# Optimization experiments

Measured on AMD Instinct MI355X. Metric: run time of the kernel, lower is better.

## Reference

```python
import jax, jax.numpy as jnp
import numpy as np

S, L, E, H, HID, T = 4096, 16, 256, 512, 512, 50
CHAR_V = 128


def _lstm_scan(x, W_ih, W_hh, b):
    """x: [T, B, D] -> all hidden states [T, B, H]. PyTorch gate order i,f,g,o.
    b is the sum of torch's b_ih + b_hh (identical math)."""
    Hh = W_hh.shape[1]
    B = x.shape[1]

    def cell(carry, xt):
        h, c = carry
        g = xt @ W_ih.T + h @ W_hh.T + b  # [B, 4H]
        i, f, gg, o = jnp.split(g, 4, axis=-1)
        c = jax.nn.sigmoid(f) * c + jax.nn.sigmoid(i) * jnp.tanh(gg)
        h = jax.nn.sigmoid(o) * jnp.tanh(c)
        return (h, c), h

    init = (jnp.zeros((B, Hh), x.dtype), jnp.zeros((B, Hh), x.dtype))
    _, hs = jax.lax.scan(cell, init, x)
    return hs


def setup_inputs() -> dict:
    key = jax.random.key(0)
    ks = jax.random.split(key, 18)

    def p(k, shape):
        return jax.random.normal(k, shape, jnp.float32) * 0.05

    return {
        "chars": jax.random.randint(ks[0], (S, L), 0, CHAR_V),
        "char_lens": jax.random.randint(ks[1], (S,), 0, L),
        "char_table": p(ks[2], (CHAR_V, E)),
        "cW_ih": p(ks[3], (4 * E, E)),
        "cW_hh": p(ks[4], (4 * E, E)),
        "cb": p(ks[5], (4 * E,)),
        "W_ih0": p(ks[6], (2, 4 * H, E)),
        "W_hh0": p(ks[7], (2, 4 * H, H)),
        "b0": p(ks[8], (2, 4 * H)),
        "W_ih1": p(ks[9], (2, 4 * H, 2 * H)),
        "W_hh1": p(ks[10], (2, 4 * H, H)),
        "b1": p(ks[11], (2, 4 * H)),
        "fc1_w": p(ks[12], (HID, 2 * H)),
        "fc1_b": p(ks[13], (HID,)),
        "fc2_w": p(ks[14], (T, HID)),
        "fc2_b": p(ks[15], (T,)),
    }


def reference(chars, char_lens, char_table, cW_ih, cW_hh, cb,
              W_ih0, W_hh0, b0, W_ih1, W_hh1, b1,
              fc1_w, fc1_b, fc2_w, fc2_b):
    n_words = chars.shape[0]
    # --- char LSTM: batched over all words (replaces per-word python loop) ---
    emb = char_table[chars]                               # [S, L, E]
    hs = _lstm_scan(emb.transpose(1, 0, 2), cW_ih, cW_hh, cb)  # [L, S, E]
    lens = jnp.maximum(char_lens, 1)                      # every word has >=1 char
    word_emb = hs[lens - 1, jnp.arange(n_words)]          # hn per word: [S, E]

    # --- 2-layer bidirectional sentence LSTM, batch = 1 ---
    x = word_emb[:, None, :]                              # [S, 1, E]

    def bi_layer(x, Wih, Whh, b):
        fwd = _lstm_scan(x, Wih[0], Whh[0], b[0])
        bwd = _lstm_scan(x[::-1], Wih[1], Whh[1], b[1])[::-1]
        return jnp.concatenate([fwd, bwd], axis=-1)       # [S, 1, 2H]

    x = bi_layer(x, W_ih0, W_hh0, b0)
    x = bi_layer(x, W_ih1, W_hh1, b1)

    # --- MLP head ---
    out = x[:, 0, :]                                      # [S, 2H]
    out = jnp.tanh(out @ fc1_w.T + fc1_b)                 # [S, HID]
    return out @ fc2_w.T + fc2_b                          # [S, T]
```

## Files before the change

kernel.cpp:

```cpp
#include <hip/hip_runtime.h>
#include <math.h>
#include <stdint.h>


#define NPOS 4096
#define GDIM 2048

__device__ __forceinline__ float sigf(float x) { return 1.0f / (1.0f + __expf(-x)); }
__device__ __forceinline__ float tanh_fast(float x) {
  float e = __expf(2.f * x);
  return 1.f - 2.f / (e + 1.f);
}

__global__ __launch_bounds__(256) void build_wt_kernel(
    const float* __restrict__ cWih, const float* __restrict__ cWhh,
    float* __restrict__ Wt)
{
  __shared__ float tile[64][65];
  const int k0 = blockIdx.x * 64;
  const int g0 = blockIdx.y * 64;
  const float* src = (k0 < 256) ? cWih : cWhh;
  const int sk0 = k0 & 255;
  for (int i = threadIdx.x; i < 64 * 64; i += 256) {
    int r = i >> 6, cc = i & 63;
    tile[r][cc] = src[(size_t)(g0 + r) * 256 + sk0 + cc];
  }
  __syncthreads();
  for (int i = threadIdx.x; i < 64 * 64; i += 256) {
    int kk = i >> 6, gg = i & 63;
    Wt[(size_t)(k0 + kk) * 1024 + g0 + gg] = tile[gg][kk];
  }
}

__global__ __launch_bounds__(256) void char_lstm_kernel(
    const int* __restrict__ chars, const int* __restrict__ lens,
    const float* __restrict__ table, const float* __restrict__ Wt,
    const float* __restrict__ cb, float* __restrict__ word_emb)
{
  __shared__ float u[16][512];
  __shared__ float wt[8][1024];
  __shared__ int sidx[16];
  const int tid = threadIdx.x;
  const int ch = tid;
  const int w0 = blockIdx.x * 16;
  if (tid < 16) { int l = lens[w0 + tid]; sidx[tid] = (l < 1 ? 1 : l) - 1; }
  float c[16], acc0[16], acc1[16], acc2[16], acc3[16];
  #pragma unroll
  for (int w = 0; w < 16; ++w) { u[w][256 + ch] = 0.f; c[w] = 0.f; }
  const float cb0 = cb[ch], cb1 = cb[256 + ch], cb2 = cb[512 + ch], cb3 = cb[768 + ch];

  for (int t = 0; t < 16; ++t) {
    for (int w = 0; w < 16; ++w) {
      int cid = chars[(w0 + w) * 16 + t];
      u[w][ch] = table[(size_t)cid * 256 + ch];
    }
    #pragma unroll
    for (int w = 0; w < 16; ++w) { acc0[w] = cb0; acc1[w] = cb1; acc2[w] = cb2; acc3[w] = cb3; }
    for (int k0 = 0; k0 < 512; k0 += 8) {
      #pragma unroll
      for (int r = 0; r < 8; ++r)
        ((float4*)&wt[r][0])[tid] = ((const float4*)(Wt + (size_t)(k0 + r) * 1024))[tid];
      __syncthreads();
      #pragma unroll
      for (int kk = 0; kk < 8; ++kk) {
        const float wv0 = wt[kk][ch], wv1 = wt[kk][256 + ch];
        const float wv2 = wt[kk][512 + ch], wv3 = wt[kk][768 + ch];
        #pragma unroll
        for (int w = 0; w < 16; ++w) {
          const float uv = u[w][k0 + kk];
          acc0[w] = fmaf(wv0, uv, acc0[w]);
          acc1[w] = fmaf(wv1, uv, acc1[w]);
          acc2[w] = fmaf(wv2, uv, acc2[w]);
          acc3[w] = fmaf(wv3, uv, acc3[w]);
        }
      }
      __syncthreads();
    }
    #pragma unroll
    for (int w = 0; w < 16; ++w) {
      float iv = sigf(acc0[w]), fv = sigf(acc1[w]);
      float gv = tanhf(acc2[w]), ov = sigf(acc3[w]);
      c[w] = fv * c[w] + iv * gv;
      float h = ov * tanhf(c[w]);
      u[w][256 + ch] = h;
      if (t == sidx[w]) word_emb[(size_t)(w0 + w) * 256 + ch] = h;
    }
  }
}

template <int SPLIT, int ACT>
__global__ __launch_bounds__(256) void gemm_kernel(
    const float* __restrict__ A, const float* __restrict__ A2,
    const float* __restrict__ B, const float* __restrict__ bias,
    float* __restrict__ C, int M, int N, int K)
{
  __shared__ float At[8][132];
  __shared__ float Bt[8][132];
  const int tid = threadIdx.x;
  const int bm0 = blockIdx.x * 128, bn0 = blockIdx.y * 128;
  float acc[8][8];
  #pragma unroll
  for (int i = 0; i < 8; ++i)
    #pragma unroll
    for (int j = 0; j < 8; ++j) acc[i][j] = 0.f;
  const int sr = tid >> 1;
  const int sk = (tid & 1) * 4;
  const int tm = (tid >> 4) * 8, tn = (tid & 15) * 8;
  for (int k0 = 0; k0 < K; k0 += 8) {
    const int kg = k0 + sk;
    float4 av;
    if (SPLIT) {
      const float* srcp = (kg < 512) ? A : A2;
      av = *(const float4*)(srcp + (size_t)(bm0 + sr) * 512 + (kg & 511));
    } else {
      av = *(const float4*)(A + (size_t)(bm0 + sr) * K + kg);
    }
    float4 bv = {0.f, 0.f, 0.f, 0.f};
    if (bn0 + sr < N) bv = *(const float4*)(B + (size_t)(bn0 + sr) * K + kg);
    At[sk + 0][sr] = av.x; At[sk + 1][sr] = av.y; At[sk + 2][sr] = av.z; At[sk + 3][sr] = av.w;
    Bt[sk + 0][sr] = bv.x; Bt[sk + 1][sr] = bv.y; Bt[sk + 2][sr] = bv.z; Bt[sk + 3][sr] = bv.w;
    __syncthreads();
    #pragma unroll
    for (int kk = 0; kk < 8; ++kk) {
      float a[8], b[8];
      *(float4*)&a[0] = *(const float4*)&At[kk][tm];
      *(float4*)&a[4] = *(const float4*)&At[kk][tm + 4];
      *(float4*)&b[0] = *(const float4*)&Bt[kk][tn];
      *(float4*)&b[4] = *(const float4*)&Bt[kk][tn + 4];
      #pragma unroll
      for (int i = 0; i < 8; ++i)
        #pragma unroll
        for (int j = 0; j < 8; ++j) acc[i][j] = fmaf(a[i], b[j], acc[i][j]);
    }
    __syncthreads();
  }
  #pragma unroll
  for (int i = 0; i < 8; ++i) {
    const int m = bm0 + tm + i;
    float* crow = C + (size_t)m * N;
    #pragma unroll
    for (int j = 0; j < 8; ++j) {
      const int n = bn0 + tn + j;
      if (n < N) {
        float v = acc[i][j] + bias[n];
        if (ACT) v = tanhf(v);
        crow[n] = v;
      }
    }
  }
}

__global__ __launch_bounds__(512) void scan_kernel(
    const float* __restrict__ Xf, const float* __restrict__ Xb,
    const float* __restrict__ Whf, const float* __restrict__ Whb,
    unsigned long long* __restrict__ Tf, unsigned long long* __restrict__ Tb,
    float* __restrict__ Hf, float* __restrict__ Hb)
{
  __shared__ float lds_h[2][576];
  const int tid = threadIdx.x;
  const int dir = blockIdx.x & 1;
  const int wg  = blockIdx.x >> 1;
  const float* X = dir ? Xb : Xf;
  const float* Wh = dir ? Whb : Whf;
  unsigned long long* T = dir ? Tb : Tf;
  float* Hd = dir ? Hb : Hf;

  const int row8 = tid >> 3;
  const int klane = tid & 7;
  const int u = row8 >> 2, g = row8 & 3;
  const int R = g * 512 + wg * 16 + u;

  float wreg[64];
  {
    const float* wrow = Wh + (size_t)R * 512 + klane * 64;
    #pragma unroll
    for (int i = 0; i < 16; ++i) {
      float4 v = ((const float4*)wrow)[i];
      wreg[4 * i] = v.x; wreg[4 * i + 1] = v.y; wreg[4 * i + 2] = v.z; wreg[4 * i + 3] = v.w;
    }
  }
  const int l0 = 72 * klane;
  const int l1 = l0 + 36;
  const int la = tid + ((tid >> 5) << 2);

  for (int i = tid; i < 576; i += 512) lds_h[0][i] = 0.f;

  const bool xl = (klane == 0);
  float xcur = 0.f, xnxt = 0.f;
  if (xl) {
    xcur = X[(size_t)(dir ? NPOS - 1 : 0) * GDIM + R];
    xnxt = X[(size_t)(dir ? NPOS - 2 : 1) * GDIM + R];
  }
  float creg = 0.f;
  __syncthreads();

  for (int s = 0; s < NPOS; ++s) {
    const int p = dir ? (NPOS - 1 - s) : s;
    if (s > 0) {
      const unsigned int tg = (unsigned int)s;
      const unsigned long long* w = T + (size_t)((s - 1) & 1) * 512 + tid;
      unsigned long long v;
      do { v = __hip_atomic_load(w, __ATOMIC_RELAXED, __HIP_MEMORY_SCOPE_AGENT); }
      while ((unsigned int)(v >> 32) != tg);
      lds_h[s & 1][la] = __uint_as_float((unsigned int)v);
    }
    __syncthreads();
    const float* hb = &lds_h[s & 1][0];
    float sum = xl ? xcur : 0.f;
    if (xl) {
      xcur = xnxt;
      if (s + 2 < NPOS) xnxt = X[(size_t)(dir ? NPOS - 3 - s : s + 2) * GDIM + R];
    }
    #pragma unroll
    for (int i = 0; i < 8; ++i) {
      float4 a = *(const float4*)&hb[l0 + 4 * i];
      sum = fmaf(wreg[4 * i + 0], a.x, sum);
      sum = fmaf(wreg[4 * i + 1], a.y, sum);
      sum = fmaf(wreg[4 * i + 2], a.z, sum);
      sum = fmaf(wreg[4 * i + 3], a.w, sum);
    }
    #pragma unroll
    for (int i = 0; i < 8; ++i) {
      float4 a = *(const float4*)&hb[l1 + 4 * i];
      sum = fmaf(wreg[32 + 4 * i + 0], a.x, sum);
      sum = fmaf(wreg[32 + 4 * i + 1], a.y, sum);
      sum = fmaf(wreg[32 + 4 * i + 2], a.z, sum);
      sum = fmaf(wreg[32 + 4 * i + 3], a.w, sum);
    }
    sum += __shfl_xor(sum, 1);
    sum += __shfl_xor(sum, 2);
    sum += __shfl_xor(sum, 4);
    const int base = (tid & 63) & ~31;
    float gf = __shfl(sum, base + 8);
    float gg = __shfl(sum, base + 16);
    float go = __shfl(sum, base + 24);
    if ((tid & 31) == 0) {
      float iv = sigf(sum), fv = sigf(gf), gv = tanh_fast(gg), ov = sigf(go);
      creg = fv * creg + iv * gv;
      float h = ov * tanh_fast(creg);
      const int j = wg * 16 + u;
      unsigned long long pack = ((unsigned long long)(unsigned int)(s + 1) << 32)
                              | (unsigned long long)__float_as_uint(h);
      __hip_atomic_store(&T[(size_t)(s & 1) * 512 + j], pack,
                         __ATOMIC_RELAXED, __HIP_MEMORY_SCOPE_AGENT);
      Hd[(size_t)p * 512 + j] = h;
    }
  }
}

extern "C" void kernel_launch(void* const* d_in, const int* in_sizes, int n_in,
                              void* d_out, int out_size, void* d_ws, size_t ws_size,
                              hipStream_t stream) {
  const int* chars = (const int*)d_in[0];
  const int* lens = (const int*)d_in[1];
  const float* table = (const float*)d_in[2];
  const float* cWih = (const float*)d_in[3];
  const float* cWhh = (const float*)d_in[4];
  const float* cb = (const float*)d_in[5];
  const float* Wih0 = (const float*)d_in[6];
  const float* Whh0 = (const float*)d_in[7];
  const float* b0 = (const float*)d_in[8];
  const float* Wih1 = (const float*)d_in[9];
  const float* Whh1 = (const float*)d_in[10];
  const float* b1 = (const float*)d_in[11];
  const float* fc1w = (const float*)d_in[12];
  const float* fc1b = (const float*)d_in[13];
  const float* fc2w = (const float*)d_in[14];
  const float* fc2b = (const float*)d_in[15];
  float* out = (float*)d_out;

  char* ws = (char*)d_ws;
  size_t off = 0;
  auto alloc = [&](size_t bytes) -> void* {
    void* p = ws + off;
    off += (bytes + 255) & ~(size_t)255;
    return p;
  };
  float* word_emb = (float*)alloc((size_t)4096 * 256 * 4);
  float* X0f = (float*)alloc((size_t)4096 * 2048 * 4);
  float* X0b = (float*)alloc((size_t)4096 * 2048 * 4);
  float* H0f = (float*)alloc((size_t)4096 * 512 * 4);
  float* H0b = (float*)alloc((size_t)4096 * 512 * 4);
  float* H1f = (float*)alloc((size_t)4096 * 512 * 4);
  float* H1b = (float*)alloc((size_t)4096 * 512 * 4);
  float* fc1out = (float*)alloc((size_t)4096 * 512 * 4);
  float* Wt = (float*)alloc((size_t)512 * 1024 * 4);
  unsigned long long* Tall = (unsigned long long*)alloc((size_t)4 * 1024 * 8);
  unsigned long long* T0f = Tall;
  unsigned long long* T0b = Tall + 1024;
  unsigned long long* T1f = Tall + 2048;
  unsigned long long* T1b = Tall + 3072;
  if (off > ws_size) return;

  hipMemsetAsync(Tall, 0, (size_t)4 * 1024 * 8, stream);

  build_wt_kernel<<<dim3(8, 16), 256, 0, stream>>>(cWih, cWhh, Wt);
  char_lstm_kernel<<<256, 256, 0, stream>>>(chars, lens, table, Wt, cb, word_emb);

  gemm_kernel<0, 0><<<dim3(32, 16), 256, 0, stream>>>(
      word_emb, nullptr, Wih0, b0, X0f, 4096, 2048, 256);
  gemm_kernel<0, 0><<<dim3(32, 16), 256, 0, stream>>>(
      word_emb, nullptr, Wih0 + (size_t)2048 * 256, b0 + 2048, X0b, 4096, 2048, 256);
  scan_kernel<<<64, 512, 0, stream>>>(X0f, X0b, Whh0, Whh0 + (size_t)2048 * 512,
                                      T0f, T0b, H0f, H0b);

  gemm_kernel<1, 0><<<dim3(32, 16), 256, 0, stream>>>(
      H0f, H0b, Wih1, b1, X0f, 4096, 2048, 1024);
  gemm_kernel<1, 0><<<dim3(32, 16), 256, 0, stream>>>(
      H0f, H0b, Wih1 + (size_t)2048 * 1024, b1 + 2048, X0b, 4096, 2048, 1024);
  scan_kernel<<<64, 512, 0, stream>>>(X0f, X0b, Whh1, Whh1 + (size_t)2048 * 512,
                                      T1f, T1b, H1f, H1b);

  gemm_kernel<1, 1><<<dim3(32, 4), 256, 0, stream>>>(
      H1f, H1b, fc1w, fc1b, fc1out, 4096, 512, 1024);
  gemm_kernel<0, 0><<<dim3(32, 1), 256, 0, stream>>>(
      fc1out, nullptr, fc2w, fc2b, out, 4096, 50, 512);
}
```

Before: 16.68 ms.

## Restructure recurrent scan into single-wave blocks with vectorized polling and permuted gate layout

The bidirectional scan kernel moves from 64 blocks of 512 threads to 512 single-wavefront blocks, each owning two hidden units. Each lane holds an 8-wide slice of the recurrent weights for all four gates in registers. It polls the previous step's hidden state with four cache-bypassing 16-byte loads and reduces across the wave with shuffles, which removes the LDS staging and __syncthreads from every step. The input-projection GEMMs write a gate-interleaved layout so each unit's four gate preactivations arrive as one float4. The trade-off is that 8x more blocks must all stay resident and spin on global memory at every step, and each step pays a full 64-lane butterfly reduction over eight accumulators.

```diff
diff --git a/kernel.cpp b/kernel.cpp
--- a/kernel.cpp
+++ b/kernel.cpp
@@ -5,6 +5,8 @@
 
 #define NPOS 4096
 #define GDIM 2048
+
+typedef unsigned int uint4v __attribute__((ext_vector_type(4)));
 
 __device__ __forceinline__ float sigf(float x) { return 1.0f / (1.0f + __expf(-x)); }
 __device__ __forceinline__ float tanh_fast(float x) {
@@ -88,7 +90,7 @@
   }
 }
 
-template <int SPLIT, int ACT>
+template <int SPLIT, int ACT, int PERM>
 __global__ __launch_bounds__(256) void gemm_kernel(
     const float* __restrict__ A, const float* __restrict__ A2,
     const float* __restrict__ B, const float* __restrict__ bias,
@@ -144,106 +146,118 @@
       if (n < N) {
         float v = acc[i][j] + bias[n];
         if (ACT) v = tanhf(v);
-        crow[n] = v;
+        if (PERM) crow[((n & 511) << 2) | (n >> 9)] = v;
+        else      crow[n] = v;
       }
     }
   }
 }
 
-__global__ __launch_bounds__(512) void scan_kernel(
+__global__ __launch_bounds__(64) void scan_kernel(
     const float* __restrict__ Xf, const float* __restrict__ Xb,
     const float* __restrict__ Whf, const float* __restrict__ Whb,
     unsigned long long* __restrict__ Tf, unsigned long long* __restrict__ Tb,
     float* __restrict__ Hf, float* __restrict__ Hb)
 {
-  __shared__ float lds_h[2][576];
-  const int tid = threadIdx.x;
-  const int dir = blockIdx.x & 1;
-  const int wg  = blockIdx.x >> 1;
+  const int bid = blockIdx.x;
+  const int dir = bid >> 8;
+  const int wg  = bid & 255;
+  const int lane = threadIdx.x;
+  const int j0 = wg * 2;
   const float* X = dir ? Xb : Xf;
   const float* Wh = dir ? Whb : Whf;
   unsigned long long* T = dir ? Tb : Tf;
   float* Hd = dir ? Hb : Hf;
 
-  const int row8 = tid >> 3;
-  const int klane = tid & 7;
-  const int u = row8 >> 2, g = row8 & 3;
-  const int R = g * 512 + wg * 16 + u;
-
-  float wreg[64];
-  {
-    const float* wrow = Wh + (size_t)R * 512 + klane * 64;
-    #pragma unroll
-    for (int i = 0; i < 16; ++i) {
-      float4 v = ((const float4*)wrow)[i];
-      wreg[4 * i] = v.x; wreg[4 * i + 1] = v.y; wreg[4 * i + 2] = v.z; wreg[4 * i + 3] = v.w;
-    }
-  }
-  const int l0 = 72 * klane;
-  const int l1 = l0 + 36;
-  const int la = tid + ((tid >> 5) << 2);
-
-  for (int i = tid; i < 576; i += 512) lds_h[0][i] = 0.f;
-
-  const bool xl = (klane == 0);
-  float xcur = 0.f, xnxt = 0.f;
-  if (xl) {
-    xcur = X[(size_t)(dir ? NPOS - 1 : 0) * GDIM + R];
-    xnxt = X[(size_t)(dir ? NPOS - 2 : 1) * GDIM + R];
+  float w[2][4][8];
+  #pragma unroll
+  for (int u = 0; u < 2; ++u)
+    #pragma unroll
+    for (int g = 0; g < 4; ++g) {
+      const float* wr = Wh + ((size_t)(g * 512 + j0 + u)) * 512 + lane * 8;
+      *(float4*)&w[u][g][0] = *(const float4*)wr;
+      *(float4*)&w[u][g][4] = *(const float4*)(wr + 4);
+    }
+
+  float4 xc = {0,0,0,0}, xn = {0,0,0,0};
+  if (lane < 2) {
+    xc = *(const float4*)&X[(size_t)(dir ? NPOS - 1 : 0) * GDIM + (j0 + lane) * 4];
+    xn = *(const float4*)&X[(size_t)(dir ? NPOS - 2 : 1) * GDIM + (j0 + lane) * 4];
   }
   float creg = 0.f;
-  __syncthreads();
 
   for (int s = 0; s < NPOS; ++s) {
     const int p = dir ? (NPOS - 1 - s) : s;
+    float s00 = 0.f, s01 = 0.f, s02 = 0.f, s03 = 0.f;
+    float s10 = 0.f, s11 = 0.f, s12 = 0.f, s13 = 0.f;
+
     if (s > 0) {
       const unsigned int tg = (unsigned int)s;
-      const unsigned long long* w = T + (size_t)((s - 1) & 1) * 512 + tid;
-      unsigned long long v;
-      do { v = __hip_atomic_load(w, __ATOMIC_RELAXED, __HIP_MEMORY_SCOPE_AGENT); }
-      while ((unsigned int)(v >> 32) != tg);
-      lds_h[s & 1][la] = __uint_as_float((unsigned int)v);
-    }
-    __syncthreads();
-    const float* hb = &lds_h[s & 1][0];
-    float sum = xl ? xcur : 0.f;
-    if (xl) {
-      xcur = xnxt;
-      if (s + 2 < NPOS) xnxt = X[(size_t)(dir ? NPOS - 3 - s : s + 2) * GDIM + R];
-    }
-    #pragma unroll
-    for (int i = 0; i < 8; ++i) {
-      float4 a = *(const float4*)&hb[l0 + 4 * i];
-      sum = fmaf(wreg[4 * i + 0], a.x, sum);
-      sum = fmaf(wreg[4 * i + 1], a.y, sum);
-      sum = fmaf(wreg[4 * i + 2], a.z, sum);
-      sum = fmaf(wreg[4 * i + 3], a.w, sum);
-    }
-    #pragma unroll
-    for (int i = 0; i < 8; ++i) {
-      float4 a = *(const float4*)&hb[l1 + 4 * i];
-      sum = fmaf(wreg[32 + 4 * i + 0], a.x, sum);
-      sum = fmaf(wreg[32 + 4 * i + 1], a.y, sum);
-      sum = fmaf(wreg[32 + 4 * i + 2], a.z, sum);
-      sum = fmaf(wreg[32 + 4 * i + 3], a.w, sum);
-    }
-    sum += __shfl_xor(sum, 1);
-    sum += __shfl_xor(sum, 2);
-    sum += __shfl_xor(sum, 4);
-    const int base = (tid & 63) & ~31;
-    float gf = __shfl(sum, base + 8);
-    float gg = __shfl(sum, base + 16);
-    float go = __shfl(sum, base + 24);
-    if ((tid & 31) == 0) {
-      float iv = sigf(sum), fv = sigf(gf), gv = tanh_fast(gg), ov = sigf(go);
+      const unsigned long long* bp = T + (size_t)((s - 1) & 1) * 512 + lane * 8;
+      uint4v q0, q1, q2, q3;
+      bool ok;
+      do {
+        asm volatile(
+            "global_load_dwordx4 %0, %4, off sc0 sc1\n\t"
+            "global_load_dwordx4 %1, %4, off offset:16 sc0 sc1\n\t"
+            "global_load_dwordx4 %2, %4, off offset:32 sc0 sc1\n\t"
+            "global_load_dwordx4 %3, %4, off offset:48 sc0 sc1\n\t"
+            "s_waitcnt vmcnt(0)"
+            : "=&v"(q0), "=&v"(q1), "=&v"(q2), "=&v"(q3)
+            : "v"(bp)
+            : "memory");
+        ok = (q0.y == tg) & (q0.w == tg) & (q1.y == tg) & (q1.w == tg)
+           & (q2.y == tg) & (q2.w == tg) & (q3.y == tg) & (q3.w == tg);
+      } while (!ok);
+      float hk[8];
+      hk[0] = __uint_as_float(q0.x); hk[1] = __uint_as_float(q0.z);
+      hk[2] = __uint_as_float(q1.x); hk[3] = __uint_as_float(q1.z);
+      hk[4] = __uint_as_float(q2.x); hk[5] = __uint_as_float(q2.z);
+      hk[6] = __uint_as_float(q3.x); hk[7] = __uint_as_float(q3.z);
+      #pragma unroll
+      for (int i = 0; i < 8; ++i) {
+        const float hv = hk[i];
+        s00 = fmaf(w[0][0][i], hv, s00);
+        s01 = fmaf(w[0][1][i], hv, s01);
+        s02 = fmaf(w[0][2][i], hv, s02);
+        s03 = fmaf(w[0][3][i], hv, s03);
+        s10 = fmaf(w[1][0][i], hv, s10);
+        s11 = fmaf(w[1][1][i], hv, s11);
+        s12 = fmaf(w[1][2][i], hv, s12);
+        s13 = fmaf(w[1][3][i], hv, s13);
+      }
+    }
+
+    float4 xnn = {0, 0, 0, 0};
+    if (lane < 2 && s + 2 < NPOS) {
+      const int p2 = dir ? (NPOS - 3 - s) : (s + 2);
+      xnn = *(const float4*)&X[(size_t)p2 * GDIM + (j0 + lane) * 4];
+    }
+
+    #pragma unroll
+    for (int m = 1; m < 64; m <<= 1) {
+      s00 += __shfl_xor(s00, m); s01 += __shfl_xor(s01, m);
+      s02 += __shfl_xor(s02, m); s03 += __shfl_xor(s03, m);
+      s10 += __shfl_xor(s10, m); s11 += __shfl_xor(s11, m);
+      s12 += __shfl_xor(s12, m); s13 += __shfl_xor(s13, m);
+    }
+
+    if (lane < 2) {
+      const float gi = (lane ? s10 : s00) + xc.x;
+      const float gf = (lane ? s11 : s01) + xc.y;
+      const float gc = (lane ? s12 : s02) + xc.z;
+      const float go = (lane ? s13 : s03) + xc.w;
+      const float iv = sigf(gi), fv = sigf(gf);
+      const float gv = tanh_fast(gc), ov = sigf(go);
       creg = fv * creg + iv * gv;
-      float h = ov * tanh_fast(creg);
-      const int j = wg * 16 + u;
+      const float h = ov * tanh_fast(creg);
+      const int j = j0 + lane;
       unsigned long long pack = ((unsigned long long)(unsigned int)(s + 1) << 32)
                               | (unsigned long long)__float_as_uint(h);
       __hip_atomic_store(&T[(size_t)(s & 1) * 512 + j], pack,
                          __ATOMIC_RELAXED, __HIP_MEMORY_SCOPE_AGENT);
       Hd[(size_t)p * 512 + j] = h;
+      xc = xn; xn = xnn;
     }
   }
 }
@@ -297,22 +311,22 @@
   build_wt_kernel<<<dim3(8, 16), 256, 0, stream>>>(cWih, cWhh, Wt);
   char_lstm_kernel<<<256, 256, 0, stream>>>(chars, lens, table, Wt, cb, word_emb);
 
-  gemm_kernel<0, 0><<<dim3(32, 16), 256, 0, stream>>>(
+  gemm_kernel<0, 0, 1><<<dim3(32, 16), 256, 0, stream>>>(
       word_emb, nullptr, Wih0, b0, X0f, 4096, 2048, 256);
-  gemm_kernel<0, 0><<<dim3(32, 16), 256, 0, stream>>>(
+  gemm_kernel<0, 0, 1><<<dim3(32, 16), 256, 0, stream>>>(
       word_emb, nullptr, Wih0 + (size_t)2048 * 256, b0 + 2048, X0b, 4096, 2048, 256);
-  scan_kernel<<<64, 512, 0, stream>>>(X0f, X0b, Whh0, Whh0 + (size_t)2048 * 512,
+  scan_kernel<<<512, 64, 0, stream>>>(X0f, X0b, Whh0, Whh0 + (size_t)2048 * 512,
                                       T0f, T0b, H0f, H0b);
 
-  gemm_kernel<1, 0><<<dim3(32, 16), 256, 0, stream>>>(
+  gemm_kernel<1, 0, 1><<<dim3(32, 16), 256, 0, stream>>>(
       H0f, H0b, Wih1, b1, X0f, 4096, 2048, 1024);
-  gemm_kernel<1, 0><<<dim3(32, 16), 256, 0, stream>>>(
+  gemm_kernel<1, 0, 1><<<dim3(32, 16), 256, 0, stream>>>(
       H0f, H0b, Wih1 + (size_t)2048 * 1024, b1 + 2048, X0b, 4096, 2048, 1024);
-  scan_kernel<<<64, 512, 0, stream>>>(X0f, X0b, Whh1, Whh1 + (size_t)2048 * 512,
+  scan_kernel<<<512, 64, 0, stream>>>(X0f, X0b, Whh1, Whh1 + (size_t)2048 * 512,
                                       T1f, T1b, H1f, H1b);
 
-  gemm_kernel<1, 1><<<dim3(32, 4), 256, 0, stream>>>(
+  gemm_kernel<1, 1, 0><<<dim3(32, 4), 256, 0, stream>>>(
       H1f, H1b, fc1w, fc1b, fc1out, 4096, 512, 1024);
-  gemm_kernel<0, 0><<<dim3(32, 1), 256, 0, stream>>>(
+  gemm_kernel<0, 0, 0><<<dim3(32, 1), 256, 0, stream>>>(
       fc1out, nullptr, fc2w, fc2b, out, 4096, 50, 512);
 }
```

After: 36.28 ms. 2.17x slower.

## Replicate scan h-exchange buffers, permute gate columns, swizzle GEMM LDS

Applied to the files above, without the earlier changes.

The scan kernel now writes each new hidden value to four replicated exchange buffers, and each workgroup polls the replica chosen by wg&3. This spreads the atomic polling traffic across more cache lines. The input-projection GEMMs write their output with gate-interleaved columns (unit*4+gate), so the scan's X reads become contiguous per workgroup instead of strided across four 512-wide gate blocks. The GEMM shared-memory tiles use a swizzled padding layout to reduce bank conflicts. In exchange, the scan does four times as many atomic stores per step and the workspace is larger.

```diff
diff --git a/kernel.cpp b/kernel.cpp
--- a/kernel.cpp
+++ b/kernel.cpp
@@ -88,14 +88,15 @@
   }
 }
 
-template <int SPLIT, int ACT>
+#define SW(c) ((c) + (((c) >> 3) << 2))
+template <int SPLIT, int ACT, int PERM>
 __global__ __launch_bounds__(256) void gemm_kernel(
     const float* __restrict__ A, const float* __restrict__ A2,
     const float* __restrict__ B, const float* __restrict__ bias,
     float* __restrict__ C, int M, int N, int K)
 {
-  __shared__ float At[8][132];
-  __shared__ float Bt[8][132];
+  __shared__ float At[8 * 192];
+  __shared__ float Bt[8 * 192];
   const int tid = threadIdx.x;
   const int bm0 = blockIdx.x * 128, bn0 = blockIdx.y * 128;
   float acc[8][8];
@@ -106,6 +107,8 @@
   const int sr = tid >> 1;
   const int sk = (tid & 1) * 4;
   const int tm = (tid >> 4) * 8, tn = (tid & 15) * 8;
+  const int swsr = SW(sr);
+  const int stm = SW(tm), stn = SW(tn);
   for (int k0 = 0; k0 < K; k0 += 8) {
     const int kg = k0 + sk;
     float4 av;
@@ -117,16 +120,18 @@
     }
     float4 bv = {0.f, 0.f, 0.f, 0.f};
     if (bn0 + sr < N) bv = *(const float4*)(B + (size_t)(bn0 + sr) * K + kg);
-    At[sk + 0][sr] = av.x; At[sk + 1][sr] = av.y; At[sk + 2][sr] = av.z; At[sk + 3][sr] = av.w;
-    Bt[sk + 0][sr] = bv.x; Bt[sk + 1][sr] = bv.y; Bt[sk + 2][sr] = bv.z; Bt[sk + 3][sr] = bv.w;
+    At[(sk + 0) * 192 + swsr] = av.x; At[(sk + 1) * 192 + swsr] = av.y;
+    At[(sk + 2) * 192 + swsr] = av.z; At[(sk + 3) * 192 + swsr] = av.w;
+    Bt[(sk + 0) * 192 + swsr] = bv.x; Bt[(sk + 1) * 192 + swsr] = bv.y;
+    Bt[(sk + 2) * 192 + swsr] = bv.z; Bt[(sk + 3) * 192 + swsr] = bv.w;
     __syncthreads();
     #pragma unroll
     for (int kk = 0; kk < 8; ++kk) {
       float a[8], b[8];
-      *(float4*)&a[0] = *(const float4*)&At[kk][tm];
-      *(float4*)&a[4] = *(const float4*)&At[kk][tm + 4];
-      *(float4*)&b[0] = *(const float4*)&Bt[kk][tn];
-      *(float4*)&b[4] = *(const float4*)&Bt[kk][tn + 4];
+      *(float4*)&a[0] = *(const float4*)&At[kk * 192 + stm];
+      *(float4*)&a[4] = *(const float4*)&At[kk * 192 + stm + 4];
+      *(float4*)&b[0] = *(const float4*)&Bt[kk * 192 + stn];
+      *(float4*)&b[4] = *(const float4*)&Bt[kk * 192 + stn + 4];
       #pragma unroll
       for (int i = 0; i < 8; ++i)
         #pragma unroll
@@ -144,7 +149,8 @@
       if (n < N) {
         float v = acc[i][j] + bias[n];
         if (ACT) v = tanhf(v);
-        crow[n] = v;
+        if (PERM) crow[((n & 511) << 2) | (n >> 9)] = v;
+        else      crow[n] = v;
       }
     }
   }
@@ -182,14 +188,16 @@
   const int l0 = 72 * klane;
   const int l1 = l0 + 36;
   const int la = tid + ((tid >> 5) << 2);
+  const int rep = wg & 3;
 
   for (int i = tid; i < 576; i += 512) lds_h[0][i] = 0.f;
 
   const bool xl = (klane == 0);
+  const int xoff = wg * 64 + row8;
   float xcur = 0.f, xnxt = 0.f;
   if (xl) {
-    xcur = X[(size_t)(dir ? NPOS - 1 : 0) * GDIM + R];
-    xnxt = X[(size_t)(dir ? NPOS - 2 : 1) * GDIM + R];
+    xcur = X[(size_t)(dir ? NPOS - 1 : 0) * GDIM + xoff];
+    xnxt = X[(size_t)(dir ? NPOS - 2 : 1) * GDIM + xoff];
   }
   float creg = 0.f;
   __syncthreads();
@@ -198,7 +206,8 @@
     const int p = dir ? (NPOS - 1 - s) : s;
     if (s > 0) {
       const unsigned int tg = (unsigned int)s;
-      const unsigned long long* w = T + (size_t)((s - 1) & 1) * 512 + tid;
+      const unsigned long long* w =
+          T + (size_t)((rep << 1) | ((s - 1) & 1)) * 512 + tid;
       unsigned long long v;
       do { v = __hip_atomic_load(w, __ATOMIC_RELAXED, __HIP_MEMORY_SCOPE_AGENT); }
       while ((unsigned int)(v >> 32) != tg);
@@ -209,7 +218,7 @@
     float sum = xl ? xcur : 0.f;
     if (xl) {
       xcur = xnxt;
-      if (s + 2 < NPOS) xnxt = X[(size_t)(dir ? NPOS - 3 - s : s + 2) * GDIM + R];
+      if (s + 2 < NPOS) xnxt = X[(size_t)(dir ? NPOS - 3 - s : s + 2) * GDIM + xoff];
     }
     #pragma unroll
     for (int i = 0; i < 8; ++i) {
@@ -241,8 +250,10 @@
       const int j = wg * 16 + u;
       unsigned long long pack = ((unsigned long long)(unsigned int)(s + 1) << 32)
                               | (unsigned long long)__float_as_uint(h);
-      __hip_atomic_store(&T[(size_t)(s & 1) * 512 + j], pack,
-                         __ATOMIC_RELAXED, __HIP_MEMORY_SCOPE_AGENT);
+      #pragma unroll
+      for (int r2 = 0; r2 < 4; ++r2)
+        __hip_atomic_store(&T[(size_t)((r2 << 1) | (s & 1)) * 512 + j], pack,
+                           __ATOMIC_RELAXED, __HIP_MEMORY_SCOPE_AGENT);
       Hd[(size_t)p * 512 + j] = h;
     }
   }
@@ -285,34 +296,34 @@
   float* H1b = (float*)alloc((size_t)4096 * 512 * 4);
   float* fc1out = (float*)alloc((size_t)4096 * 512 * 4);
   float* Wt = (float*)alloc((size_t)512 * 1024 * 4);
-  unsigned long long* Tall = (unsigned long long*)alloc((size_t)4 * 1024 * 8);
+  unsigned long long* Tall = (unsigned long long*)alloc((size_t)4 * 4096 * 8);
   unsigned long long* T0f = Tall;
-  unsigned long long* T0b = Tall + 1024;
-  unsigned long long* T1f = Tall + 2048;
-  unsigned long long* T1b = Tall + 3072;
+  unsigned long long* T0b = Tall + 4096;
+  unsigned long long* T1f = Tall + 8192;
+  unsigned long long* T1b = Tall + 12288;
   if (off > ws_size) return;
 
-  hipMemsetAsync(Tall, 0, (size_t)4 * 1024 * 8, stream);
+  hipMemsetAsync(Tall, 0, (size_t)4 * 4096 * 8, stream);
 
   build_wt_kernel<<<dim3(8, 16), 256, 0, stream>>>(cWih, cWhh, Wt);
   char_lstm_kernel<<<256, 256, 0, stream>>>(chars, lens, table, Wt, cb, word_emb);
 
-  gemm_kernel<0, 0><<<dim3(32, 16), 256, 0, stream>>>(
+  gemm_kernel<0, 0, 1><<<dim3(32, 16), 256, 0, stream>>>(
       word_emb, nullptr, Wih0, b0, X0f, 4096, 2048, 256);
-  gemm_kernel<0, 0><<<dim3(32, 16), 256, 0, stream>>>(
+  gemm_kernel<0, 0, 1><<<dim3(32, 16), 256, 0, stream>>>(
       word_emb, nullptr, Wih0 + (size_t)2048 * 256, b0 + 2048, X0b, 4096, 2048, 256);
   scan_kernel<<<64, 512, 0, stream>>>(X0f, X0b, Whh0, Whh0 + (size_t)2048 * 512,
                                       T0f, T0b, H0f, H0b);
 
-  gemm_kernel<1, 0><<<dim3(32, 16), 256, 0, stream>>>(
+  gemm_kernel<1, 0, 1><<<dim3(32, 16), 256, 0, stream>>>(
       H0f, H0b, Wih1, b1, X0f, 4096, 2048, 1024);
-  gemm_kernel<1, 0><<<dim3(32, 16), 256, 0, stream>>>(
+  gemm_kernel<1, 0, 1><<<dim3(32, 16), 256, 0, stream>>>(
       H0f, H0b, Wih1 + (size_t)2048 * 1024, b1 + 2048, X0b, 4096, 2048, 1024);
   scan_kernel<<<64, 512, 0, stream>>>(X0f, X0b, Whh1, Whh1 + (size_t)2048 * 512,
                                       T1f, T1b, H1f, H1b);
 
-  gemm_kernel<1, 1><<<dim3(32, 4), 256, 0, stream>>>(
+  gemm_kernel<1, 1, 0><<<dim3(32, 4), 256, 0, stream>>>(
       H1f, H1b, fc1w, fc1b, fc1out, 4096, 512, 1024);
-  gemm_kernel<0, 0><<<dim3(32, 1), 256, 0, stream>>>(
+  gemm_kernel<0, 0, 0><<<dim3(32, 1), 256, 0, stream>>>(
       fc1out, nullptr, fc2w, fc2b, out, 4096, 50, 512);
 }
```

After: 16.52 ms. No clear change (-1.0%).
